# Performance work log

Measured on AMD Instinct MI355X. Metric: run time of the kernel, lower is better.

The kernel has to match this reference:

```python
import jax, jax.numpy as jnp
import numpy as np

T, H = 4096, 7168          # tokens, hidden size
Q_LORA, KV_LORA = 1536, 512
ROPE, NOPE, NH = 64, 128, 16
QK = NOPE + ROPE
MAXPOS, SLOTS = 8192, 16384
EPS = 1e-6


def _build_cos_sin_cache():
    # rotary cache layout used by the module: [max_pos, rope] = cos_half || sin_half
    half = ROPE // 2
    inv_freq = 1.0 / (10000.0 ** (np.arange(0, half, dtype=np.float32) / half))
    t = np.arange(MAXPOS, dtype=np.float32)
    freqs = np.outer(t, inv_freq)  # [MAXPOS, half]
    return jnp.asarray(np.concatenate([np.cos(freqs), np.sin(freqs)], axis=-1))


def setup_inputs() -> dict:
    key = jax.random.key(0)
    ks = jax.random.split(key, 8)
    return {
        "hidden_states": jax.random.normal(ks[0], (T, H), jnp.float32),
        "positions": jax.random.randint(ks[1], (T,), 0, MAXPOS, jnp.int32),
        "w_qkv_a": jax.random.normal(ks[2], (H, Q_LORA + KV_LORA + ROPE), jnp.float32) * 0.02,
        "q_a_ln_w": jnp.ones((Q_LORA,), jnp.float32),
        "w_q_b": jax.random.normal(ks[3], (Q_LORA, NH * QK), jnp.float32) * 0.02,
        "kv_a_ln_w": jnp.ones((KV_LORA,), jnp.float32),
        "w_kc": jax.random.normal(ks[4], (NH, NOPE, KV_LORA), jnp.float32) * 0.02,
        "cos_sin_cache": _build_cos_sin_cache(),
        "k_cache": jnp.zeros((SLOTS, KV_LORA), jnp.float32),
        "rope_cache": jnp.zeros((SLOTS, ROPE), jnp.float32),
        "slot_mapping": jnp.arange(T, dtype=jnp.int32),
    }


def _rms_norm(x, w, eps=EPS):
    return x * jax.lax.rsqrt(jnp.mean(x * x, axis=-1, keepdims=True) + eps) * w


def _interleave_rope(x, cos, sin):
    # npu_interleave_rope: de-interleave even/odd lanes into halves, then
    # apply neox-style rotation with full-dim (repeated) cos/sin.
    x1 = x[..., 0::2]
    x2 = x[..., 1::2]
    rot = jnp.concatenate([x1, x2], axis=-1)
    h = rot.shape[-1] // 2
    rot_half = jnp.concatenate([-rot[..., h:], rot[..., :h]], axis=-1)
    return rot * cos + rot_half * sin


def reference(hidden_states, positions, w_qkv_a, q_a_ln_w, w_q_b, kv_a_ln_w,
              w_kc, cos_sin_cache, k_cache, rope_cache, slot_mapping):
    # get_sin_cos: gather cache, chunk in halves, repeat each to full rope dim
    cs = cos_sin_cache[positions]                 # [T, ROPE]
    cos, sin = jnp.split(cs, 2, axis=-1)          # [T, ROPE/2] each
    cos = jnp.tile(cos, (1, 2))                   # [T, ROPE]
    sin = jnp.tile(sin, (1, 2))

    # fused qkv_a projection -> q low-rank + latent kv cache
    qkv = hidden_states @ w_qkv_a                 # [T, Q_LORA + KV_LORA + ROPE]
    q_low = qkv[:, :Q_LORA]
    latent = qkv[:, Q_LORA:]

    # q path: RMSNorm -> q_b projection -> per-head split
    q = _rms_norm(q_low, q_a_ln_w)
    q = (q @ w_q_b).reshape(-1, NH, QK)           # [T, NH, QK]
    q_nope, q_pe = q[..., :NOPE], q[..., NOPE:]

    # absorb: q_nope @ w_kc per head -> [T, NH, KV_LORA]
    q_nope = jnp.einsum("thn,hnk->thk", q_nope, w_kc)
    # interleaved rope on q_pe
    q_pe = _interleave_rope(q_pe, cos[:, None, :], sin[:, None, :])

    # kv path (npu_kv_rmsnorm_rope_cache): rmsnorm latent, rope the rope part,
    # scatter both into the paged caches at slot_mapping
    k_nope = _rms_norm(latent[:, :KV_LORA], kv_a_ln_w)     # [T, KV_LORA]
    k_rope = _interleave_rope(latent[:, KV_LORA:], cos, sin)  # [T, ROPE]
    k_cache = k_cache.at[slot_mapping].set(k_nope)
    rope_cache = rope_cache.at[slot_mapping].set(k_rope)

    q_out = jnp.concatenate([q_nope, q_pe], axis=-1)       # [T, NH, KV_LORA+ROPE]
    k_out = jnp.concatenate([k_nope, k_rope], axis=-1)     # [T, KV_LORA+ROPE]
    return q_out, k_out, k_cache, rope_cache
```

## Files before the change

kernel.cpp:

```cpp
#include <hip/hip_runtime.h>
#include <hip/hip_bf16.h>

typedef __bf16 bf16_t;
typedef __bf16 bf16x4 __attribute__((ext_vector_type(4)));
typedef __bf16 bf16x8 __attribute__((ext_vector_type(8)));
typedef float f32x4 __attribute__((ext_vector_type(4)));
typedef unsigned int uint;

#define T_TOK 4096
#define H_DIM 7168
#define QLORA 1536
#define KVLORA 512
#define ROPE_D 64
#define NOPE_D 128
#define NHEAD 16
#define NQKV 2112
#define NQB  3072
#define EPS_F 1e-6f


__global__ void cast_f32_bf16(const float* __restrict__ in, bf16_t* __restrict__ out, long n8)
{
    long stride = (long)gridDim.x * blockDim.x;
    for (long i = (long)blockIdx.x * blockDim.x + threadIdx.x; i < n8; i += stride) {
        const float4 a = ((const float4*)in)[i * 2];
        const float4 b = ((const float4*)in)[i * 2 + 1];
        bf16x8 v;
        v[0] = (bf16_t)a.x; v[1] = (bf16_t)a.y; v[2] = (bf16_t)a.z; v[3] = (bf16_t)a.w;
        v[4] = (bf16_t)b.x; v[5] = (bf16_t)b.y; v[6] = (bf16_t)b.z; v[7] = (bf16_t)b.w;
        ((bf16x8*)out)[i] = v;
    }
}

__global__ __launch_bounds__(256) void transpose_cast64(const float* __restrict__ in,
                                                        bf16_t* __restrict__ out, int R, int C)
{
    __shared__ float tile[64][65];
    const int bx = blockIdx.x * 64;
    const int by = blockIdx.y * 64;
    const int tx = threadIdx.x & 15, ty = threadIdx.x >> 4;
    #pragma unroll
    for (int i = 0; i < 4; i++) {
        const int r = ty + 16 * i;
        const float4 v = *(const float4*)&in[(long)(by + r) * C + bx + tx * 4];
        tile[r][tx * 4 + 0] = v.x; tile[r][tx * 4 + 1] = v.y;
        tile[r][tx * 4 + 2] = v.z; tile[r][tx * 4 + 3] = v.w;
    }
    __syncthreads();
    #pragma unroll
    for (int i = 0; i < 4; i++) {
        const int cc = ty + 16 * i;
        bf16x4 o;
        o[0] = (bf16_t)tile[tx * 4 + 0][cc];
        o[1] = (bf16_t)tile[tx * 4 + 1][cc];
        o[2] = (bf16_t)tile[tx * 4 + 2][cc];
        o[3] = (bf16_t)tile[tx * 4 + 3][cc];
        *(bf16x4*)&out[(long)(bx + cc) * R + by + tx * 4] = o;
    }
}

__device__ inline float block_sum_256(float v)
{
    #pragma unroll
    for (int off = 32; off > 0; off >>= 1) v += __shfl_xor(v, off, 64);
    __shared__ float tmp[4];
    __syncthreads();
    if ((threadIdx.x & 63) == 0) tmp[threadIdx.x >> 6] = v;
    __syncthreads();
    return tmp[0] + tmp[1] + tmp[2] + tmp[3];
}

__global__ __launch_bounds__(256) void rmsq_kside_kernel(
    const float* __restrict__ qkv, const float* __restrict__ qB,
    const float* __restrict__ qC, const float* __restrict__ qD,
    const float* __restrict__ q_w, const float* __restrict__ kv_w,
    const float* __restrict__ cos_sin, const int* __restrict__ positions,
    const int* __restrict__ slot_map,
    bf16_t* __restrict__ q_a, float* __restrict__ k_out,
    float* __restrict__ kc_out, float* __restrict__ rc_out)
{
    const int t = blockIdx.x;
    const long base = (long)t * NQKV;
    const float* x = qkv + base;
    const float* xB = qB ? qB + base : nullptr;
    const float* xC = qC ? qC + base : nullptr;
    const float* xD = qD ? qD + base : nullptr;

    float loc[6];
    float ss = 0.f;
    #pragma unroll
    for (int i = 0; i < 6; i++) {
        int idx = threadIdx.x + 256 * i;
        float v = x[idx];
        if (xB) v += xB[idx];
        if (xC) v += xC[idx];
        if (xD) v += xD[idx];
        loc[i] = v; ss += v * v;
    }
    ss = block_sum_256(ss);
    const float scq = rsqrtf(ss / (float)QLORA + EPS_F);
    #pragma unroll
    for (int i = 0; i < 6; i++) {
        int idx = threadIdx.x + 256 * i;
        q_a[(long)t * QLORA + idx] = (bf16_t)(loc[i] * scq * q_w[idx]);
    }

    float v0 = x[QLORA + threadIdx.x];
    float v1 = x[QLORA + threadIdx.x + 256];
    if (xB) { v0 += xB[QLORA + threadIdx.x]; v1 += xB[QLORA + threadIdx.x + 256]; }
    if (xC) { v0 += xC[QLORA + threadIdx.x]; v1 += xC[QLORA + threadIdx.x + 256]; }
    if (xD) { v0 += xD[QLORA + threadIdx.x]; v1 += xD[QLORA + threadIdx.x + 256]; }
    float ssk = v0 * v0 + v1 * v1;
    ssk = block_sum_256(ssk);
    const float sck = rsqrtf(ssk / (float)KVLORA + EPS_F);
    const int slot = slot_map[t];
    const float a0 = v0 * sck * kv_w[threadIdx.x];
    const float a1 = v1 * sck * kv_w[threadIdx.x + 256];
    k_out[(long)t * 576 + threadIdx.x]        = a0;
    k_out[(long)t * 576 + 256 + threadIdx.x]  = a1;
    kc_out[(long)slot * KVLORA + threadIdx.x]       = a0;
    kc_out[(long)slot * KVLORA + 256 + threadIdx.x] = a1;
    if (threadIdx.x < 32) {
        const int j = threadIdx.x;
        const int pos = positions[t];
        const float c = cos_sin[pos * 64 + j];
        const float s = cos_sin[pos * 64 + 32 + j];
        float x1 = x[QLORA + KVLORA + 2 * j];
        float x2 = x[QLORA + KVLORA + 2 * j + 1];
        if (xB) { x1 += xB[QLORA + KVLORA + 2 * j]; x2 += xB[QLORA + KVLORA + 2 * j + 1]; }
        if (xC) { x1 += xC[QLORA + KVLORA + 2 * j]; x2 += xC[QLORA + KVLORA + 2 * j + 1]; }
        if (xD) { x1 += xD[QLORA + KVLORA + 2 * j]; x2 += xD[QLORA + KVLORA + 2 * j + 1]; }
        const float o1 = x1 * c - x2 * s;
        const float o2 = x2 * c + x1 * s;
        k_out[(long)t * 576 + 512 + j]      = o1;
        k_out[(long)t * 576 + 512 + 32 + j] = o2;
        rc_out[(long)slot * 64 + j]      = o1;
        rc_out[(long)slot * 64 + 32 + j] = o2;
    }
}

#define GBM 128
#define GBN 128
#define GBK 64

__global__ __launch_bounds__(512) void gemm_mfma(
    const bf16_t* __restrict__ A, int lda, long sA,
    const bf16_t* __restrict__ Bt, int ldb, long sB,
    float* __restrict__ C, int ldc, long sC,
    int K, int N)
{
    __shared__ bf16_t As[2][GBM * GBK];
    __shared__ bf16_t Bs[2][GBN * GBK];

    const int nwg = gridDim.x * gridDim.y;
    const int bid = blockIdx.y * gridDim.x + blockIdx.x;
    const int cpx = nwg >> 3;
    const int swz = (bid & 7) * cpx + (bid >> 3);
    const int bx = swz % gridDim.x;
    const int by = swz / gridDim.x;

    const int tid = threadIdx.x;
    const int lane = tid & 63;
    const int w = tid >> 6;
    const int wr = w >> 2, wc = w & 3;
    const int fr = lane & 15;
    const int kg = lane >> 4;

    const long brow = (long)by * GBM;
    const long bcol = (long)bx * GBN;

    const bf16_t* Ab = A + blockIdx.z * sA + brow * lda;
    const bf16_t* Bb = Bt + blockIdx.z * sB;
    float* Cb = C + blockIdx.z * sC + brow * ldc;

    const int srow = w * 16 + (lane >> 3);
    const int scol = (((lane & 7) ^ (lane >> 3)) * 8);

    const uint rd_sw = (uint)((kg * 16) ^ ((fr & 7) << 4));
    const uint a_base = (uint)(uintptr_t)(&As[0][0]) + (uint)((wr * 64 + fr) * 128) + rd_sw;
    const uint b_base = (uint)(uintptr_t)(&Bs[0][0]) + (uint)((wc * 32 + fr) * 128) + rd_sw;

    f32x4 acc[4][2] = {};

    const int nt = K / GBK;

    auto stage = [&](int buf, int k0) {
        #pragma unroll
        for (int it = 0; it < 2; it++) {
            const int r = srow + it * 8;
            __builtin_amdgcn_global_load_lds(
                (const __attribute__((address_space(1))) void*)(Ab + (long)r * lda + k0 + scol),
                (__attribute__((address_space(3))) void*)(&As[buf][(w * 16 + it * 8) * GBK]),
                16, 0, 0);
        }
        #pragma unroll
        for (int it = 0; it < 2; it++) {
            const int r = srow + it * 8;
            long bn = bcol + r; if (bn >= N) bn = N - 1;
            __builtin_amdgcn_global_load_lds(
                (const __attribute__((address_space(1))) void*)(Bb + bn * ldb + k0 + scol),
                (__attribute__((address_space(3))) void*)(&Bs[buf][(w * 16 + it * 8) * GBK]),
                16, 0, 0);
        }
    };

    stage(0, 0);
    asm volatile("s_waitcnt vmcnt(0)" ::: "memory");
    __builtin_amdgcn_s_barrier();

    int cur = 0;
    for (int t = 0; t < nt; ++t) {
        if (t + 1 < nt) stage(cur ^ 1, (t + 1) * GBK);

        const uint aa  = a_base + (uint)(cur * (GBM * GBK * 2));
        const uint bb  = b_base + (uint)(cur * (GBN * GBK * 2));
        const uint aaX = aa ^ 64u;
        const uint bbX = bb ^ 64u;
        bf16x8 a00, a01, a02, a03, a10, a11, a12, a13, b00, b01, b10, b11;
        asm volatile("ds_read_b128 %0, %1 offset:0"    : "=v"(a00) : "v"(aa));
        asm volatile("ds_read_b128 %0, %1 offset:2048" : "=v"(a01) : "v"(aa));
        asm volatile("ds_read_b128 %0, %1 offset:4096" : "=v"(a02) : "v"(aa));
        asm volatile("ds_read_b128 %0, %1 offset:6144" : "=v"(a03) : "v"(aa));
        asm volatile("ds_read_b128 %0, %1 offset:0"    : "=v"(a10) : "v"(aaX));
        asm volatile("ds_read_b128 %0, %1 offset:2048" : "=v"(a11) : "v"(aaX));
        asm volatile("ds_read_b128 %0, %1 offset:4096" : "=v"(a12) : "v"(aaX));
        asm volatile("ds_read_b128 %0, %1 offset:6144" : "=v"(a13) : "v"(aaX));
        asm volatile("ds_read_b128 %0, %1 offset:0"    : "=v"(b00) : "v"(bb));
        asm volatile("ds_read_b128 %0, %1 offset:2048" : "=v"(b01) : "v"(bb));
        asm volatile("ds_read_b128 %0, %1 offset:0"    : "=v"(b10) : "v"(bbX));
        asm volatile("ds_read_b128 %0, %1 offset:2048" : "=v"(b11) : "v"(bbX));
        asm volatile("s_waitcnt lgkmcnt(0)" ::: "memory");
        __builtin_amdgcn_sched_barrier(0);

        acc[0][0] = __builtin_amdgcn_mfma_f32_16x16x32_bf16(a00, b00, acc[0][0], 0, 0, 0);
        acc[0][1] = __builtin_amdgcn_mfma_f32_16x16x32_bf16(a00, b01, acc[0][1], 0, 0, 0);
        acc[1][0] = __builtin_amdgcn_mfma_f32_16x16x32_bf16(a01, b00, acc[1][0], 0, 0, 0);
        acc[1][1] = __builtin_amdgcn_mfma_f32_16x16x32_bf16(a01, b01, acc[1][1], 0, 0, 0);
        acc[2][0] = __builtin_amdgcn_mfma_f32_16x16x32_bf16(a02, b00, acc[2][0], 0, 0, 0);
        acc[2][1] = __builtin_amdgcn_mfma_f32_16x16x32_bf16(a02, b01, acc[2][1], 0, 0, 0);
        acc[3][0] = __builtin_amdgcn_mfma_f32_16x16x32_bf16(a03, b00, acc[3][0], 0, 0, 0);
        acc[3][1] = __builtin_amdgcn_mfma_f32_16x16x32_bf16(a03, b01, acc[3][1], 0, 0, 0);
        acc[0][0] = __builtin_amdgcn_mfma_f32_16x16x32_bf16(a10, b10, acc[0][0], 0, 0, 0);
        acc[0][1] = __builtin_amdgcn_mfma_f32_16x16x32_bf16(a10, b11, acc[0][1], 0, 0, 0);
        acc[1][0] = __builtin_amdgcn_mfma_f32_16x16x32_bf16(a11, b10, acc[1][0], 0, 0, 0);
        acc[1][1] = __builtin_amdgcn_mfma_f32_16x16x32_bf16(a11, b11, acc[1][1], 0, 0, 0);
        acc[2][0] = __builtin_amdgcn_mfma_f32_16x16x32_bf16(a12, b10, acc[2][0], 0, 0, 0);
        acc[2][1] = __builtin_amdgcn_mfma_f32_16x16x32_bf16(a12, b11, acc[2][1], 0, 0, 0);
        acc[3][0] = __builtin_amdgcn_mfma_f32_16x16x32_bf16(a13, b10, acc[3][0], 0, 0, 0);
        acc[3][1] = __builtin_amdgcn_mfma_f32_16x16x32_bf16(a13, b11, acc[3][1], 0, 0, 0);

        asm volatile("s_waitcnt vmcnt(0)" ::: "memory");
        __builtin_amdgcn_s_barrier();
        cur ^= 1;
    }

    #pragma unroll
    for (int i = 0; i < 4; i++) {
        #pragma unroll
        for (int j = 0; j < 2; j++) {
            const int row0 = wr * 64 + i * 16 + kg * 4;
            const long col = bcol + wc * 32 + j * 16 + fr;
            if (col < N) {
                #pragma unroll
                for (int r = 0; r < 4; r++)
                    Cb[(long)(row0 + r) * ldc + col] = acc[i][j][r];
            }
        }
    }
}

__global__ __launch_bounds__(512) void gemm2_fused(
    const bf16_t* __restrict__ A,
    const bf16_t* __restrict__ Bt,
    const float* __restrict__ cos_sin,
    const int* __restrict__ positions,
    bf16_t* __restrict__ q_nope,
    float* __restrict__ q_out)
{
    __shared__ bf16_t As[2][GBM * GBK];
    __shared__ bf16_t Bs[2][GBN * GBK];

    const int nwg = gridDim.x * gridDim.y;
    const int bid = blockIdx.y * gridDim.x + blockIdx.x;
    const int cpx = nwg >> 3;
    const int swz = (bid & 7) * cpx + (bid >> 3);
    const int bx = swz % gridDim.x;
    const int by = swz / gridDim.x;

    const int tid = threadIdx.x;
    const int lane = tid & 63;
    const int w = tid >> 6;
    const int wr = w >> 2, wc = w & 3;
    const int fr = lane & 15;
    const int kg = lane >> 4;

    const int brow = by * GBM;
    const int bcol = bx * GBN;

    const bf16_t* Ab = A + (long)brow * QLORA;
    const bf16_t* Bb = Bt + (long)bcol * QLORA;

    const int srow = w * 16 + (lane >> 3);
    const int scol = (((lane & 7) ^ (lane >> 3)) * 8);

    const uint rd_sw = (uint)((kg * 16) ^ ((fr & 7) << 4));
    const uint a_base = (uint)(uintptr_t)(&As[0][0]) + (uint)((wr * 64 + fr) * 128) + rd_sw;
    const uint b_base = (uint)(uintptr_t)(&Bs[0][0]) + (uint)((wc * 32 + fr) * 128) + rd_sw;

    f32x4 acc[4][2] = {};

    const int nt = QLORA / GBK;

    auto stage = [&](int buf, int k0) {
        #pragma unroll
        for (int it = 0; it < 2; it++) {
            const int r = srow + it * 8;
            __builtin_amdgcn_global_load_lds(
                (const __attribute__((address_space(1))) void*)(Ab + (long)r * QLORA + k0 + scol),
                (__attribute__((address_space(3))) void*)(&As[buf][(w * 16 + it * 8) * GBK]),
                16, 0, 0);
            __builtin_amdgcn_global_load_lds(
                (const __attribute__((address_space(1))) void*)(Bb + (long)r * QLORA + k0 + scol),
                (__attribute__((address_space(3))) void*)(&Bs[buf][(w * 16 + it * 8) * GBK]),
                16, 0, 0);
        }
    };

    stage(0, 0);
    asm volatile("s_waitcnt vmcnt(0)" ::: "memory");
    __builtin_amdgcn_s_barrier();

    int cur = 0;
    for (int t = 0; t < nt; ++t) {
        if (t + 1 < nt) stage(cur ^ 1, (t + 1) * GBK);

        const uint aa  = a_base + (uint)(cur * (GBM * GBK * 2));
        const uint bb  = b_base + (uint)(cur * (GBN * GBK * 2));
        const uint aaX = aa ^ 64u;
        const uint bbX = bb ^ 64u;
        bf16x8 a00, a01, a02, a03, a10, a11, a12, a13, b00, b01, b10, b11;
        asm volatile("ds_read_b128 %0, %1 offset:0"    : "=v"(a00) : "v"(aa));
        asm volatile("ds_read_b128 %0, %1 offset:2048" : "=v"(a01) : "v"(aa));
        asm volatile("ds_read_b128 %0, %1 offset:4096" : "=v"(a02) : "v"(aa));
        asm volatile("ds_read_b128 %0, %1 offset:6144" : "=v"(a03) : "v"(aa));
        asm volatile("ds_read_b128 %0, %1 offset:0"    : "=v"(a10) : "v"(aaX));
        asm volatile("ds_read_b128 %0, %1 offset:2048" : "=v"(a11) : "v"(aaX));
        asm volatile("ds_read_b128 %0, %1 offset:4096" : "=v"(a12) : "v"(aaX));
        asm volatile("ds_read_b128 %0, %1 offset:6144" : "=v"(a13) : "v"(aaX));
        asm volatile("ds_read_b128 %0, %1 offset:0"    : "=v"(b00) : "v"(bb));
        asm volatile("ds_read_b128 %0, %1 offset:2048" : "=v"(b01) : "v"(bb));
        asm volatile("ds_read_b128 %0, %1 offset:0"    : "=v"(b10) : "v"(bbX));
        asm volatile("ds_read_b128 %0, %1 offset:2048" : "=v"(b11) : "v"(bbX));
        asm volatile("s_waitcnt lgkmcnt(0)" ::: "memory");
        __builtin_amdgcn_sched_barrier(0);

        acc[0][0] = __builtin_amdgcn_mfma_f32_16x16x32_bf16(a00, b00, acc[0][0], 0, 0, 0);
        acc[0][1] = __builtin_amdgcn_mfma_f32_16x16x32_bf16(a00, b01, acc[0][1], 0, 0, 0);
        acc[1][0] = __builtin_amdgcn_mfma_f32_16x16x32_bf16(a01, b00, acc[1][0], 0, 0, 0);
        acc[1][1] = __builtin_amdgcn_mfma_f32_16x16x32_bf16(a01, b01, acc[1][1], 0, 0, 0);
        acc[2][0] = __builtin_amdgcn_mfma_f32_16x16x32_bf16(a02, b00, acc[2][0], 0, 0, 0);
        acc[2][1] = __builtin_amdgcn_mfma_f32_16x16x32_bf16(a02, b01, acc[2][1], 0, 0, 0);
        acc[3][0] = __builtin_amdgcn_mfma_f32_16x16x32_bf16(a03, b00, acc[3][0], 0, 0, 0);
        acc[3][1] = __builtin_amdgcn_mfma_f32_16x16x32_bf16(a03, b01, acc[3][1], 0, 0, 0);
        acc[0][0] = __builtin_amdgcn_mfma_f32_16x16x32_bf16(a10, b10, acc[0][0], 0, 0, 0);
        acc[0][1] = __builtin_amdgcn_mfma_f32_16x16x32_bf16(a10, b11, acc[0][1], 0, 0, 0);
        acc[1][0] = __builtin_amdgcn_mfma_f32_16x16x32_bf16(a11, b10, acc[1][0], 0, 0, 0);
        acc[1][1] = __builtin_amdgcn_mfma_f32_16x16x32_bf16(a11, b11, acc[1][1], 0, 0, 0);
        acc[2][0] = __builtin_amdgcn_mfma_f32_16x16x32_bf16(a12, b10, acc[2][0], 0, 0, 0);
        acc[2][1] = __builtin_amdgcn_mfma_f32_16x16x32_bf16(a12, b11, acc[2][1], 0, 0, 0);
        acc[3][0] = __builtin_amdgcn_mfma_f32_16x16x32_bf16(a13, b10, acc[3][0], 0, 0, 0);
        acc[3][1] = __builtin_amdgcn_mfma_f32_16x16x32_bf16(a13, b11, acc[3][1], 0, 0, 0);

        asm volatile("s_waitcnt vmcnt(0)" ::: "memory");
        __builtin_amdgcn_s_barrier();
        cur ^= 1;
    }

    #pragma unroll
    for (int i = 0; i < 4; i++) {
        #pragma unroll
        for (int j = 0; j < 2; j++) {
            const int row0 = wr * 64 + i * 16 + kg * 4;
            const int col  = bcol + wc * 32 + j * 16 + fr;
            const int h  = col / 192;
            const int jj = col - h * 192;
            if (jj < 128) {
                #pragma unroll
                for (int r = 0; r < 4; r++) {
                    const int t = brow + row0 + r;
                    q_nope[((long)h * T_TOK + t) * NOPE_D + jj] = (bf16_t)acc[i][j][r];
                }
            } else {
                const int idx = jj - 128;
                const int j2 = idx >> 1;
                const int odd = idx & 1;
                #pragma unroll
                for (int r = 0; r < 4; r++) {
                    const int t = brow + row0 + r;
                    const float v = acc[i][j][r];
                    const float p = __shfl_xor(v, 1, 64);
                    const int pos = positions[t];
                    const float c = cos_sin[pos * 64 + j2];
                    const float s = cos_sin[pos * 64 + 32 + j2];
                    const float o = odd ? (v * c + p * s) : (v * c - p * s);
                    q_out[(long)t * 9216 + h * 576 + 512 + (odd ? 32 : 0) + j2] = o;
                }
            }
        }
    }
}

__global__ __launch_bounds__(512) void gemm3_k128(
    const bf16_t* __restrict__ A,
    const bf16_t* __restrict__ Bt,
    float* __restrict__ C)
{
    __shared__ bf16_t As[2][GBM * GBK];
    __shared__ bf16_t Bs[2][GBN * GBK];

    const int nwg = gridDim.x * gridDim.y;
    const int bid = blockIdx.y * gridDim.x + blockIdx.x;
    const int cpx = nwg >> 3;
    const int swz = (bid & 7) * cpx + (bid >> 3);
    const int bx = swz % gridDim.x;
    const int by = swz / gridDim.x;

    const int tid = threadIdx.x;
    const int lane = tid & 63;
    const int w = tid >> 6;
    const int wr = w >> 2, wc = w & 3;
    const int fr = lane & 15;
    const int kg = lane >> 4;

    const long brow = (long)by * GBM;
    const long bcol = (long)bx * GBN;

    const bf16_t* Ab = A + (long)blockIdx.z * T_TOK * NOPE_D + brow * NOPE_D;
    const bf16_t* Bb = Bt + blockIdx.z * 128;
    float* Cb = C + blockIdx.z * 576 + brow * 9216;

    const int srow = w * 16 + (lane >> 3);
    const int scol = (((lane & 7) ^ (lane >> 3)) * 8);

    const uint rd_sw = (uint)((kg * 16) ^ ((fr & 7) << 4));

    #pragma unroll
    for (int kh = 0; kh < 2; kh++) {
        #pragma unroll
        for (int it = 0; it < 2; it++) {
            const int r = srow + it * 8;
            __builtin_amdgcn_global_load_lds(
                (const __attribute__((address_space(1))) void*)(Ab + (long)r * NOPE_D + kh * 64 + scol),
                (__attribute__((address_space(3))) void*)(&As[kh][(w * 16 + it * 8) * GBK]),
                16, 0, 0);
        }
        #pragma unroll
        for (int it = 0; it < 2; it++) {
            const int r = srow + it * 8;
            __builtin_amdgcn_global_load_lds(
                (const __attribute__((address_space(1))) void*)(Bb + (bcol + r) * 2048 + kh * 64 + scol),
                (__attribute__((address_space(3))) void*)(&Bs[kh][(w * 16 + it * 8) * GBK]),
                16, 0, 0);
        }
    }
    asm volatile("s_waitcnt vmcnt(0)" ::: "memory");
    __builtin_amdgcn_s_barrier();

    f32x4 acc[4][2] = {};

    #pragma unroll
    for (int kh = 0; kh < 2; kh++) {
        const uint aa  = (uint)(uintptr_t)(&As[kh][0]) + (uint)((wr * 64 + fr) * 128) + rd_sw;
        const uint bb  = (uint)(uintptr_t)(&Bs[kh][0]) + (uint)((wc * 32 + fr) * 128) + rd_sw;
        const uint aaX = aa ^ 64u;
        const uint bbX = bb ^ 64u;
        bf16x8 a00, a01, a02, a03, a10, a11, a12, a13, b00, b01, b10, b11;
        asm volatile("ds_read_b128 %0, %1 offset:0"    : "=v"(a00) : "v"(aa));
        asm volatile("ds_read_b128 %0, %1 offset:2048" : "=v"(a01) : "v"(aa));
        asm volatile("ds_read_b128 %0, %1 offset:4096" : "=v"(a02) : "v"(aa));
        asm volatile("ds_read_b128 %0, %1 offset:6144" : "=v"(a03) : "v"(aa));
        asm volatile("ds_read_b128 %0, %1 offset:0"    : "=v"(a10) : "v"(aaX));
        asm volatile("ds_read_b128 %0, %1 offset:2048" : "=v"(a11) : "v"(aaX));
        asm volatile("ds_read_b128 %0, %1 offset:4096" : "=v"(a12) : "v"(aaX));
        asm volatile("ds_read_b128 %0, %1 offset:6144" : "=v"(a13) : "v"(aaX));
        asm volatile("ds_read_b128 %0, %1 offset:0"    : "=v"(b00) : "v"(bb));
        asm volatile("ds_read_b128 %0, %1 offset:2048" : "=v"(b01) : "v"(bb));
        asm volatile("ds_read_b128 %0, %1 offset:0"    : "=v"(b10) : "v"(bbX));
        asm volatile("ds_read_b128 %0, %1 offset:2048" : "=v"(b11) : "v"(bbX));
        asm volatile("s_waitcnt lgkmcnt(0)" ::: "memory");
        __builtin_amdgcn_sched_barrier(0);

        acc[0][0] = __builtin_amdgcn_mfma_f32_16x16x32_bf16(a00, b00, acc[0][0], 0, 0, 0);
        acc[0][1] = __builtin_amdgcn_mfma_f32_16x16x32_bf16(a00, b01, acc[0][1], 0, 0, 0);
        acc[1][0] = __builtin_amdgcn_mfma_f32_16x16x32_bf16(a01, b00, acc[1][0], 0, 0, 0);
        acc[1][1] = __builtin_amdgcn_mfma_f32_16x16x32_bf16(a01, b01, acc[1][1], 0, 0, 0);
        acc[2][0] = __builtin_amdgcn_mfma_f32_16x16x32_bf16(a02, b00, acc[2][0], 0, 0, 0);
        acc[2][1] = __builtin_amdgcn_mfma_f32_16x16x32_bf16(a02, b01, acc[2][1], 0, 0, 0);
        acc[3][0] = __builtin_amdgcn_mfma_f32_16x16x32_bf16(a03, b00, acc[3][0], 0, 0, 0);
        acc[3][1] = __builtin_amdgcn_mfma_f32_16x16x32_bf16(a03, b01, acc[3][1], 0, 0, 0);
        acc[0][0] = __builtin_amdgcn_mfma_f32_16x16x32_bf16(a10, b10, acc[0][0], 0, 0, 0);
        acc[0][1] = __builtin_amdgcn_mfma_f32_16x16x32_bf16(a10, b11, acc[0][1], 0, 0, 0);
        acc[1][0] = __builtin_amdgcn_mfma_f32_16x16x32_bf16(a11, b10, acc[1][0], 0, 0, 0);
        acc[1][1] = __builtin_amdgcn_mfma_f32_16x16x32_bf16(a11, b11, acc[1][1], 0, 0, 0);
        acc[2][0] = __builtin_amdgcn_mfma_f32_16x16x32_bf16(a12, b10, acc[2][0], 0, 0, 0);
        acc[2][1] = __builtin_amdgcn_mfma_f32_16x16x32_bf16(a12, b11, acc[2][1], 0, 0, 0);
        acc[3][0] = __builtin_amdgcn_mfma_f32_16x16x32_bf16(a13, b10, acc[3][0], 0, 0, 0);
        acc[3][1] = __builtin_amdgcn_mfma_f32_16x16x32_bf16(a13, b11, acc[3][1], 0, 0, 0);
    }

    #pragma unroll
    for (int i = 0; i < 4; i++) {
        #pragma unroll
        for (int j = 0; j < 2; j++) {
            const int row0 = wr * 64 + i * 16 + kg * 4;
            const long col = bcol + wc * 32 + j * 16 + fr;
            #pragma unroll
            for (int r = 0; r < 4; r++)
                Cb[(long)(row0 + r) * 9216 + col] = acc[i][j][r];
        }
    }
}


extern "C" void kernel_launch(void* const* d_in, const int* in_sizes, int n_in,
                              void* d_out, int out_size, void* d_ws, size_t ws_size,
                              hipStream_t stream)
{
    const float* hs       = (const float*)d_in[0];
    const int*   positions= (const int*)d_in[1];
    const float* w_qkv_a  = (const float*)d_in[2];
    const float* q_a_ln_w = (const float*)d_in[3];
    const float* w_q_b    = (const float*)d_in[4];
    const float* kv_a_ln_w= (const float*)d_in[5];
    const float* w_kc     = (const float*)d_in[6];
    const float* cos_sin  = (const float*)d_in[7];
    const float* k_cache_in  = (const float*)d_in[8];
    const float* rope_cache_in = (const float*)d_in[9];
    const int*   slot_map = (const int*)d_in[10];

    float* out   = (float*)d_out;
    float* q_out = out;
    float* k_out = out + 37748736;
    float* kc_out = out + 40108032;
    float* rc_out = out + 48496640;

    char* ws = (char*)d_ws;
    bf16_t* hs_bf  = (bf16_t*)(ws + 0);
    bf16_t* wqkvaT = (bf16_t*)(ws + 58720256);
    bf16_t* wqbT   = (bf16_t*)(ws + 88997888);
    bf16_t* wkcT   = (bf16_t*)(ws + 98435072);
    float*  qkv0   = (float*)(ws + 100532224);

    int splitk = 1;
    if (ws_size >= (size_t)238944256) splitk = 4;
    else if (ws_size >= (size_t)169738240) splitk = 2;

    float* qkv1 = nullptr; float* qkv2 = nullptr; float* qkv3 = nullptr;
    bf16_t* q_a;
    bf16_t* q_nope;
    if (splitk >= 2) {
        qkv1   = (float*)(ws + 135135232);
        q_a    = (bf16_t*)(ws + 0);
        q_nope = (bf16_t*)(ws + 135135232);
        if (splitk == 4) {
            qkv2 = (float*)(ws + 169738240);
            qkv3 = (float*)(ws + 204341248);
        }
    } else {
        q_a    = (bf16_t*)(ws + 135135232);
        q_nope = (bf16_t*)(ws + 100532224);
    }

    hipMemcpyAsync(kc_out, k_cache_in, (size_t)16384 * 512 * 4, hipMemcpyDeviceToDevice, stream);
    hipMemcpyAsync(rc_out, rope_cache_in, (size_t)16384 * 64 * 4, hipMemcpyDeviceToDevice, stream);

    cast_f32_bf16<<<2048, 256, 0, stream>>>(hs, hs_bf, (long)T_TOK * H_DIM / 8);
    transpose_cast64<<<dim3(NQKV / 64, H_DIM / 64), 256, 0, stream>>>(w_qkv_a, wqkvaT, H_DIM, NQKV);
    transpose_cast64<<<dim3(NQB / 64, QLORA / 64), 256, 0, stream>>>(w_q_b, wqbT, QLORA, NQB);
    transpose_cast64<<<dim3(512 / 64, 2048 / 64), 256, 0, stream>>>(w_kc, wkcT, 2048, 512);

    {
        const int kslice = H_DIM / splitk;
        gemm_mfma<<<dim3((NQKV + GBN - 1) / GBN, T_TOK / GBM, splitk), 512, 0, stream>>>(
            hs_bf, H_DIM, kslice, wqkvaT, H_DIM, kslice,
            qkv0, NQKV, (long)T_TOK * NQKV, kslice, NQKV);
    }

    rmsq_kside_kernel<<<T_TOK, 256, 0, stream>>>(qkv0, qkv1, qkv2, qkv3,
                                                 q_a_ln_w, kv_a_ln_w,
                                                 cos_sin, positions, slot_map,
                                                 q_a, k_out, kc_out, rc_out);

    gemm2_fused<<<dim3(NQB / GBN, T_TOK / GBM), 512, 0, stream>>>(
        q_a, wqbT, cos_sin, positions, q_nope, q_out);

    gemm3_k128<<<dim3(KVLORA / GBN, T_TOK / GBM, NHEAD), 512, 0, stream>>>(
        q_nope, wkcT, q_out);
}
```

Before: 373.5 us.

## Use intra-block K-split wave pairs with 64x64 warp tiles in GEMMs

The QKV and q_b GEMMs now have each wave pair split the K=64 tile: both waves own a 64x64 output quadrant, and each takes half the K dimension. Partial sums are reduced through LDS before the epilogue. This gives a larger per-wave MFMA tile with fewer LDS reads per FLOP. Global split-K for the first GEMM is capped at 2, which drops the 4-way partial buffers from the RMSNorm kernel. The trade-offs are more accumulator registers (launch bounds now hint 4 blocks), an extra LDS reduction and barrier, and less parallelism for the first GEMM when the workspace would have allowed split 4.

```diff
diff --git a/kernel.cpp b/kernel.cpp
--- a/kernel.cpp
+++ b/kernel.cpp
@@ -72,7 +72,6 @@
 
 __global__ __launch_bounds__(256) void rmsq_kside_kernel(
     const float* __restrict__ qkv, const float* __restrict__ qB,
-    const float* __restrict__ qC, const float* __restrict__ qD,
     const float* __restrict__ q_w, const float* __restrict__ kv_w,
     const float* __restrict__ cos_sin, const int* __restrict__ positions,
     const int* __restrict__ slot_map,
@@ -83,8 +82,6 @@
     const long base = (long)t * NQKV;
     const float* x = qkv + base;
     const float* xB = qB ? qB + base : nullptr;
-    const float* xC = qC ? qC + base : nullptr;
-    const float* xD = qD ? qD + base : nullptr;
 
     float loc[6];
     float ss = 0.f;
@@ -93,8 +90,6 @@
         int idx = threadIdx.x + 256 * i;
         float v = x[idx];
         if (xB) v += xB[idx];
-        if (xC) v += xC[idx];
-        if (xD) v += xD[idx];
         loc[i] = v; ss += v * v;
     }
     ss = block_sum_256(ss);
@@ -108,8 +103,6 @@
     float v0 = x[QLORA + threadIdx.x];
     float v1 = x[QLORA + threadIdx.x + 256];
     if (xB) { v0 += xB[QLORA + threadIdx.x]; v1 += xB[QLORA + threadIdx.x + 256]; }
-    if (xC) { v0 += xC[QLORA + threadIdx.x]; v1 += xC[QLORA + threadIdx.x + 256]; }
-    if (xD) { v0 += xD[QLORA + threadIdx.x]; v1 += xD[QLORA + threadIdx.x + 256]; }
     float ssk = v0 * v0 + v1 * v1;
     ssk = block_sum_256(ssk);
     const float sck = rsqrtf(ssk / (float)KVLORA + EPS_F);
@@ -128,8 +121,6 @@
         float x1 = x[QLORA + KVLORA + 2 * j];
         float x2 = x[QLORA + KVLORA + 2 * j + 1];
         if (xB) { x1 += xB[QLORA + KVLORA + 2 * j]; x2 += xB[QLORA + KVLORA + 2 * j + 1]; }
-        if (xC) { x1 += xC[QLORA + KVLORA + 2 * j]; x2 += xC[QLORA + KVLORA + 2 * j + 1]; }
-        if (xD) { x1 += xD[QLORA + KVLORA + 2 * j]; x2 += xD[QLORA + KVLORA + 2 * j + 1]; }
         const float o1 = x1 * c - x2 * s;
         const float o2 = x2 * c + x1 * s;
         k_out[(long)t * 576 + 512 + j]      = o1;
@@ -143,7 +134,36 @@
 #define GBN 128
 #define GBK 64
 
-__global__ __launch_bounds__(512) void gemm_mfma(
+#define KSPLIT_TILE_COMPUTE(aa, bb)                                                          \
+    bf16x8 a0, a1, a2, a3, b0, b1, b2, b3;                                                   \
+    asm volatile("ds_read_b128 %0, %1 offset:0"    : "=v"(a0) : "v"(aa));                    \
+    asm volatile("ds_read_b128 %0, %1 offset:2048" : "=v"(a1) : "v"(aa));                    \
+    asm volatile("ds_read_b128 %0, %1 offset:4096" : "=v"(a2) : "v"(aa));                    \
+    asm volatile("ds_read_b128 %0, %1 offset:6144" : "=v"(a3) : "v"(aa));                    \
+    asm volatile("ds_read_b128 %0, %1 offset:0"    : "=v"(b0) : "v"(bb));                    \
+    asm volatile("ds_read_b128 %0, %1 offset:2048" : "=v"(b1) : "v"(bb));                    \
+    asm volatile("ds_read_b128 %0, %1 offset:4096" : "=v"(b2) : "v"(bb));                    \
+    asm volatile("ds_read_b128 %0, %1 offset:6144" : "=v"(b3) : "v"(bb));                    \
+    asm volatile("s_waitcnt lgkmcnt(0)" ::: "memory");                                       \
+    __builtin_amdgcn_sched_barrier(0);                                                       \
+    acc[0][0] = __builtin_amdgcn_mfma_f32_16x16x32_bf16(a0, b0, acc[0][0], 0, 0, 0);         \
+    acc[0][1] = __builtin_amdgcn_mfma_f32_16x16x32_bf16(a0, b1, acc[0][1], 0, 0, 0);         \
+    acc[0][2] = __builtin_amdgcn_mfma_f32_16x16x32_bf16(a0, b2, acc[0][2], 0, 0, 0);         \
+    acc[0][3] = __builtin_amdgcn_mfma_f32_16x16x32_bf16(a0, b3, acc[0][3], 0, 0, 0);         \
+    acc[1][0] = __builtin_amdgcn_mfma_f32_16x16x32_bf16(a1, b0, acc[1][0], 0, 0, 0);         \
+    acc[1][1] = __builtin_amdgcn_mfma_f32_16x16x32_bf16(a1, b1, acc[1][1], 0, 0, 0);         \
+    acc[1][2] = __builtin_amdgcn_mfma_f32_16x16x32_bf16(a1, b2, acc[1][2], 0, 0, 0);         \
+    acc[1][3] = __builtin_amdgcn_mfma_f32_16x16x32_bf16(a1, b3, acc[1][3], 0, 0, 0);         \
+    acc[2][0] = __builtin_amdgcn_mfma_f32_16x16x32_bf16(a2, b0, acc[2][0], 0, 0, 0);         \
+    acc[2][1] = __builtin_amdgcn_mfma_f32_16x16x32_bf16(a2, b1, acc[2][1], 0, 0, 0);         \
+    acc[2][2] = __builtin_amdgcn_mfma_f32_16x16x32_bf16(a2, b2, acc[2][2], 0, 0, 0);         \
+    acc[2][3] = __builtin_amdgcn_mfma_f32_16x16x32_bf16(a2, b3, acc[2][3], 0, 0, 0);         \
+    acc[3][0] = __builtin_amdgcn_mfma_f32_16x16x32_bf16(a3, b0, acc[3][0], 0, 0, 0);         \
+    acc[3][1] = __builtin_amdgcn_mfma_f32_16x16x32_bf16(a3, b1, acc[3][1], 0, 0, 0);         \
+    acc[3][2] = __builtin_amdgcn_mfma_f32_16x16x32_bf16(a3, b2, acc[3][2], 0, 0, 0);         \
+    acc[3][3] = __builtin_amdgcn_mfma_f32_16x16x32_bf16(a3, b3, acc[3][3], 0, 0, 0);
+
+__global__ __launch_bounds__(512, 4) void gemm_mfma(
     const bf16_t* __restrict__ A, int lda, long sA,
     const bf16_t* __restrict__ Bt, int ldb, long sB,
     float* __restrict__ C, int ldc, long sC,
@@ -162,7 +182,9 @@
     const int tid = threadIdx.x;
     const int lane = tid & 63;
     const int w = tid >> 6;
-    const int wr = w >> 2, wc = w & 3;
+    const int q = w >> 1;
+    const int p = w & 1;
+    const int qr = q >> 1, qc = q & 1;
     const int fr = lane & 15;
     const int kg = lane >> 4;
 
@@ -176,11 +198,11 @@
     const int srow = w * 16 + (lane >> 3);
     const int scol = (((lane & 7) ^ (lane >> 3)) * 8);
 
-    const uint rd_sw = (uint)((kg * 16) ^ ((fr & 7) << 4));
-    const uint a_base = (uint)(uintptr_t)(&As[0][0]) + (uint)((wr * 64 + fr) * 128) + rd_sw;
-    const uint b_base = (uint)(uintptr_t)(&Bs[0][0]) + (uint)((wc * 32 + fr) * 128) + rd_sw;
-
-    f32x4 acc[4][2] = {};
+    const uint rd_sw = (uint)(((kg * 16) ^ ((fr & 7) << 4)) ^ (p << 6));
+    const uint a_base = (uint)(uintptr_t)(&As[0][0]) + (uint)((qr * 64 + fr) * 128) + rd_sw;
+    const uint b_base = (uint)(uintptr_t)(&Bs[0][0]) + (uint)((qc * 64 + fr) * 128) + rd_sw;
+
+    f32x4 acc[4][4] = {};
 
     const int nt = K / GBK;
 
@@ -212,64 +234,44 @@
     for (int t = 0; t < nt; ++t) {
         if (t + 1 < nt) stage(cur ^ 1, (t + 1) * GBK);
 
-        const uint aa  = a_base + (uint)(cur * (GBM * GBK * 2));
-        const uint bb  = b_base + (uint)(cur * (GBN * GBK * 2));
-        const uint aaX = aa ^ 64u;
-        const uint bbX = bb ^ 64u;
-        bf16x8 a00, a01, a02, a03, a10, a11, a12, a13, b00, b01, b10, b11;
-        asm volatile("ds_read_b128 %0, %1 offset:0"    : "=v"(a00) : "v"(aa));
-        asm volatile("ds_read_b128 %0, %1 offset:2048" : "=v"(a01) : "v"(aa));
-        asm volatile("ds_read_b128 %0, %1 offset:4096" : "=v"(a02) : "v"(aa));
-        asm volatile("ds_read_b128 %0, %1 offset:6144" : "=v"(a03) : "v"(aa));
-        asm volatile("ds_read_b128 %0, %1 offset:0"    : "=v"(a10) : "v"(aaX));
-        asm volatile("ds_read_b128 %0, %1 offset:2048" : "=v"(a11) : "v"(aaX));
-        asm volatile("ds_read_b128 %0, %1 offset:4096" : "=v"(a12) : "v"(aaX));
-        asm volatile("ds_read_b128 %0, %1 offset:6144" : "=v"(a13) : "v"(aaX));
-        asm volatile("ds_read_b128 %0, %1 offset:0"    : "=v"(b00) : "v"(bb));
-        asm volatile("ds_read_b128 %0, %1 offset:2048" : "=v"(b01) : "v"(bb));
-        asm volatile("ds_read_b128 %0, %1 offset:0"    : "=v"(b10) : "v"(bbX));
-        asm volatile("ds_read_b128 %0, %1 offset:2048" : "=v"(b11) : "v"(bbX));
-        asm volatile("s_waitcnt lgkmcnt(0)" ::: "memory");
-        __builtin_amdgcn_sched_barrier(0);
-
-        acc[0][0] = __builtin_amdgcn_mfma_f32_16x16x32_bf16(a00, b00, acc[0][0], 0, 0, 0);
-        acc[0][1] = __builtin_amdgcn_mfma_f32_16x16x32_bf16(a00, b01, acc[0][1], 0, 0, 0);
-        acc[1][0] = __builtin_amdgcn_mfma_f32_16x16x32_bf16(a01, b00, acc[1][0], 0, 0, 0);
-        acc[1][1] = __builtin_amdgcn_mfma_f32_16x16x32_bf16(a01, b01, acc[1][1], 0, 0, 0);
-        acc[2][0] = __builtin_amdgcn_mfma_f32_16x16x32_bf16(a02, b00, acc[2][0], 0, 0, 0);
-        acc[2][1] = __builtin_amdgcn_mfma_f32_16x16x32_bf16(a02, b01, acc[2][1], 0, 0, 0);
-        acc[3][0] = __builtin_amdgcn_mfma_f32_16x16x32_bf16(a03, b00, acc[3][0], 0, 0, 0);
-        acc[3][1] = __builtin_amdgcn_mfma_f32_16x16x32_bf16(a03, b01, acc[3][1], 0, 0, 0);
-        acc[0][0] = __builtin_amdgcn_mfma_f32_16x16x32_bf16(a10, b10, acc[0][0], 0, 0, 0);
-        acc[0][1] = __builtin_amdgcn_mfma_f32_16x16x32_bf16(a10, b11, acc[0][1], 0, 0, 0);
-        acc[1][0] = __builtin_amdgcn_mfma_f32_16x16x32_bf16(a11, b10, acc[1][0], 0, 0, 0);
-        acc[1][1] = __builtin_amdgcn_mfma_f32_16x16x32_bf16(a11, b11, acc[1][1], 0, 0, 0);
-        acc[2][0] = __builtin_amdgcn_mfma_f32_16x16x32_bf16(a12, b10, acc[2][0], 0, 0, 0);
-        acc[2][1] = __builtin_amdgcn_mfma_f32_16x16x32_bf16(a12, b11, acc[2][1], 0, 0, 0);
-        acc[3][0] = __builtin_amdgcn_mfma_f32_16x16x32_bf16(a13, b10, acc[3][0], 0, 0, 0);
-        acc[3][1] = __builtin_amdgcn_mfma_f32_16x16x32_bf16(a13, b11, acc[3][1], 0, 0, 0);
+        const uint aa = a_base + (uint)(cur * (GBM * GBK * 2));
+        const uint bb = b_base + (uint)(cur * (GBN * GBK * 2));
+        { KSPLIT_TILE_COMPUTE(aa, bb) }
 
         asm volatile("s_waitcnt vmcnt(0)" ::: "memory");
         __builtin_amdgcn_s_barrier();
         cur ^= 1;
     }
 
-    #pragma unroll
-    for (int i = 0; i < 4; i++) {
-        #pragma unroll
-        for (int j = 0; j < 2; j++) {
-            const int row0 = wr * 64 + i * 16 + kg * 4;
-            const long col = bcol + wc * 32 + j * 16 + fr;
-            if (col < N) {
-                #pragma unroll
-                for (int r = 0; r < 4; r++)
-                    Cb[(long)(row0 + r) * ldc + col] = acc[i][j][r];
+    float* red = (q < 2) ? (float*)&As[0][0] : (float*)&Bs[0][0];
+    red += (q & 1) * 4096;
+    if (p == 1) {
+        #pragma unroll
+        for (int i = 0; i < 4; i++)
+            #pragma unroll
+            for (int j = 0; j < 4; j++)
+                *(f32x4*)&red[(i * 4 + j) * 256 + lane * 4] = acc[i][j];
+    }
+    __syncthreads();
+    if (p == 0) {
+        #pragma unroll
+        for (int i = 0; i < 4; i++) {
+            #pragma unroll
+            for (int j = 0; j < 4; j++) {
+                acc[i][j] += *(const f32x4*)&red[(i * 4 + j) * 256 + lane * 4];
+                const int row0 = qr * 64 + i * 16 + kg * 4;
+                const long col = bcol + qc * 64 + j * 16 + fr;
+                if (col < N) {
+                    #pragma unroll
+                    for (int r = 0; r < 4; r++)
+                        Cb[(long)(row0 + r) * ldc + col] = acc[i][j][r];
+                }
             }
         }
     }
 }
 
-__global__ __launch_bounds__(512) void gemm2_fused(
+__global__ __launch_bounds__(512, 4) void gemm2_fused(
     const bf16_t* __restrict__ A,
     const bf16_t* __restrict__ Bt,
     const float* __restrict__ cos_sin,
@@ -290,7 +292,9 @@
     const int tid = threadIdx.x;
     const int lane = tid & 63;
     const int w = tid >> 6;
-    const int wr = w >> 2, wc = w & 3;
+    const int q = w >> 1;
+    const int p = w & 1;
+    const int qr = q >> 1, qc = q & 1;
     const int fr = lane & 15;
     const int kg = lane >> 4;
 
@@ -303,11 +307,11 @@
     const int srow = w * 16 + (lane >> 3);
     const int scol = (((lane & 7) ^ (lane >> 3)) * 8);
 
-    const uint rd_sw = (uint)((kg * 16) ^ ((fr & 7) << 4));
-    const uint a_base = (uint)(uintptr_t)(&As[0][0]) + (uint)((wr * 64 + fr) * 128) + rd_sw;
-    const uint b_base = (uint)(uintptr_t)(&Bs[0][0]) + (uint)((wc * 32 + fr) * 128) + rd_sw;
-
-    f32x4 acc[4][2] = {};
+    const uint rd_sw = (uint)(((kg * 16) ^ ((fr & 7) << 4)) ^ (p << 6));
+    const uint a_base = (uint)(uintptr_t)(&As[0][0]) + (uint)((qr * 64 + fr) * 128) + rd_sw;
+    const uint b_base = (uint)(uintptr_t)(&Bs[0][0]) + (uint)((qc * 64 + fr) * 128) + rd_sw;
+
+    f32x4 acc[4][4] = {};
 
     const int nt = QLORA / GBK;
 
@@ -334,76 +338,56 @@
     for (int t = 0; t < nt; ++t) {
         if (t + 1 < nt) stage(cur ^ 1, (t + 1) * GBK);
 
-        const uint aa  = a_base + (uint)(cur * (GBM * GBK * 2));
-        const uint bb  = b_base + (uint)(cur * (GBN * GBK * 2));
-        const uint aaX = aa ^ 64u;
-        const uint bbX = bb ^ 64u;
-        bf16x8 a00, a01, a02, a03, a10, a11, a12, a13, b00, b01, b10, b11;
-        asm volatile("ds_read_b128 %0, %1 offset:0"    : "=v"(a00) : "v"(aa));
-        asm volatile("ds_read_b128 %0, %1 offset:2048" : "=v"(a01) : "v"(aa));
-        asm volatile("ds_read_b128 %0, %1 offset:4096" : "=v"(a02) : "v"(aa));
-        asm volatile("ds_read_b128 %0, %1 offset:6144" : "=v"(a03) : "v"(aa));
-        asm volatile("ds_read_b128 %0, %1 offset:0"    : "=v"(a10) : "v"(aaX));
-        asm volatile("ds_read_b128 %0, %1 offset:2048" : "=v"(a11) : "v"(aaX));
-        asm volatile("ds_read_b128 %0, %1 offset:4096" : "=v"(a12) : "v"(aaX));
-        asm volatile("ds_read_b128 %0, %1 offset:6144" : "=v"(a13) : "v"(aaX));
-        asm volatile("ds_read_b128 %0, %1 offset:0"    : "=v"(b00) : "v"(bb));
-        asm volatile("ds_read_b128 %0, %1 offset:2048" : "=v"(b01) : "v"(bb));
-        asm volatile("ds_read_b128 %0, %1 offset:0"    : "=v"(b10) : "v"(bbX));
-        asm volatile("ds_read_b128 %0, %1 offset:2048" : "=v"(b11) : "v"(bbX));
-        asm volatile("s_waitcnt lgkmcnt(0)" ::: "memory");
-        __builtin_amdgcn_sched_barrier(0);
-
-        acc[0][0] = __builtin_amdgcn_mfma_f32_16x16x32_bf16(a00, b00, acc[0][0], 0, 0, 0);
-        acc[0][1] = __builtin_amdgcn_mfma_f32_16x16x32_bf16(a00, b01, acc[0][1], 0, 0, 0);
-        acc[1][0] = __builtin_amdgcn_mfma_f32_16x16x32_bf16(a01, b00, acc[1][0], 0, 0, 0);
-        acc[1][1] = __builtin_amdgcn_mfma_f32_16x16x32_bf16(a01, b01, acc[1][1], 0, 0, 0);
-        acc[2][0] = __builtin_amdgcn_mfma_f32_16x16x32_bf16(a02, b00, acc[2][0], 0, 0, 0);
-        acc[2][1] = __builtin_amdgcn_mfma_f32_16x16x32_bf16(a02, b01, acc[2][1], 0, 0, 0);
-        acc[3][0] = __builtin_amdgcn_mfma_f32_16x16x32_bf16(a03, b00, acc[3][0], 0, 0, 0);
-        acc[3][1] = __builtin_amdgcn_mfma_f32_16x16x32_bf16(a03, b01, acc[3][1], 0, 0, 0);
-        acc[0][0] = __builtin_amdgcn_mfma_f32_16x16x32_bf16(a10, b10, acc[0][0], 0, 0, 0);
-        acc[0][1] = __builtin_amdgcn_mfma_f32_16x16x32_bf16(a10, b11, acc[0][1], 0, 0, 0);
-        acc[1][0] = __builtin_amdgcn_mfma_f32_16x16x32_bf16(a11, b10, acc[1][0], 0, 0, 0);
-        acc[1][1] = __builtin_amdgcn_mfma_f32_16x16x32_bf16(a11, b11, acc[1][1], 0, 0, 0);
-        acc[2][0] = __builtin_amdgcn_mfma_f32_16x16x32_bf16(a12, b10, acc[2][0], 0, 0, 0);
-        acc[2][1] = __builtin_amdgcn_mfma_f32_16x16x32_bf16(a12, b11, acc[2][1], 0, 0, 0);
-        acc[3][0] = __builtin_amdgcn_mfma_f32_16x16x32_bf16(a13, b10, acc[3][0], 0, 0, 0);
-        acc[3][1] = __builtin_amdgcn_mfma_f32_16x16x32_bf16(a13, b11, acc[3][1], 0, 0, 0);
+        const uint aa = a_base + (uint)(cur * (GBM * GBK * 2));
+        const uint bb = b_base + (uint)(cur * (GBN * GBK * 2));
+        { KSPLIT_TILE_COMPUTE(aa, bb) }
 
         asm volatile("s_waitcnt vmcnt(0)" ::: "memory");
         __builtin_amdgcn_s_barrier();
         cur ^= 1;
     }
 
-    #pragma unroll
-    for (int i = 0; i < 4; i++) {
-        #pragma unroll
-        for (int j = 0; j < 2; j++) {
-            const int row0 = wr * 64 + i * 16 + kg * 4;
-            const int col  = bcol + wc * 32 + j * 16 + fr;
-            const int h  = col / 192;
-            const int jj = col - h * 192;
-            if (jj < 128) {
-                #pragma unroll
-                for (int r = 0; r < 4; r++) {
-                    const int t = brow + row0 + r;
-                    q_nope[((long)h * T_TOK + t) * NOPE_D + jj] = (bf16_t)acc[i][j][r];
-                }
-            } else {
-                const int idx = jj - 128;
-                const int j2 = idx >> 1;
-                const int odd = idx & 1;
-                #pragma unroll
-                for (int r = 0; r < 4; r++) {
-                    const int t = brow + row0 + r;
-                    const float v = acc[i][j][r];
-                    const float p = __shfl_xor(v, 1, 64);
-                    const int pos = positions[t];
-                    const float c = cos_sin[pos * 64 + j2];
-                    const float s = cos_sin[pos * 64 + 32 + j2];
-                    const float o = odd ? (v * c + p * s) : (v * c - p * s);
-                    q_out[(long)t * 9216 + h * 576 + 512 + (odd ? 32 : 0) + j2] = o;
+    float* red = (q < 2) ? (float*)&As[0][0] : (float*)&Bs[0][0];
+    red += (q & 1) * 4096;
+    if (p == 1) {
+        #pragma unroll
+        for (int i = 0; i < 4; i++)
+            #pragma unroll
+            for (int j = 0; j < 4; j++)
+                *(f32x4*)&red[(i * 4 + j) * 256 + lane * 4] = acc[i][j];
+    }
+    __syncthreads();
+    if (p == 0) {
+        #pragma unroll
+        for (int i = 0; i < 4; i++) {
+            #pragma unroll
+            for (int j = 0; j < 4; j++) {
+                acc[i][j] += *(const f32x4*)&red[(i * 4 + j) * 256 + lane * 4];
+                const int row0 = qr * 64 + i * 16 + kg * 4;
+                const int col  = bcol + qc * 64 + j * 16 + fr;
+                const int h  = col / 192;
+                const int jj = col - h * 192;
+                if (jj < 128) {
+                    #pragma unroll
+                    for (int r = 0; r < 4; r++) {
+                        const int t = brow + row0 + r;
+                        q_nope[((long)h * T_TOK + t) * NOPE_D + jj] = (bf16_t)acc[i][j][r];
+                    }
+                } else {
+                    const int idx = jj - 128;
+                    const int j2 = idx >> 1;
+                    const int odd = idx & 1;
+                    #pragma unroll
+                    for (int r = 0; r < 4; r++) {
+                        const int t = brow + row0 + r;
+                        const float v = acc[i][j][r];
+                        const float pr = __shfl_xor(v, 1, 64);
+                        const int pos = positions[t];
+                        const float c = cos_sin[pos * 64 + j2];
+                        const float s = cos_sin[pos * 64 + 32 + j2];
+                        const float o = odd ? (v * c + pr * s) : (v * c - pr * s);
+                        q_out[(long)t * 9216 + h * 576 + 512 + (odd ? 32 : 0) + j2] = o;
+                    }
                 }
             }
         }
@@ -551,21 +535,15 @@
     bf16_t* wkcT   = (bf16_t*)(ws + 98435072);
     float*  qkv0   = (float*)(ws + 100532224);
 
-    int splitk = 1;
-    if (ws_size >= (size_t)238944256) splitk = 4;
-    else if (ws_size >= (size_t)169738240) splitk = 2;
-
-    float* qkv1 = nullptr; float* qkv2 = nullptr; float* qkv3 = nullptr;
+    const bool splitk = ws_size >= (size_t)169738240;
+
+    float* qkv1 = nullptr;
     bf16_t* q_a;
     bf16_t* q_nope;
-    if (splitk >= 2) {
+    if (splitk) {
         qkv1   = (float*)(ws + 135135232);
         q_a    = (bf16_t*)(ws + 0);
         q_nope = (bf16_t*)(ws + 135135232);
-        if (splitk == 4) {
-            qkv2 = (float*)(ws + 169738240);
-            qkv3 = (float*)(ws + 204341248);
-        }
     } else {
         q_a    = (bf16_t*)(ws + 135135232);
         q_nope = (bf16_t*)(ws + 100532224);
@@ -579,15 +557,16 @@
     transpose_cast64<<<dim3(NQB / 64, QLORA / 64), 256, 0, stream>>>(w_q_b, wqbT, QLORA, NQB);
     transpose_cast64<<<dim3(512 / 64, 2048 / 64), 256, 0, stream>>>(w_kc, wkcT, 2048, 512);
 
-    {
-        const int kslice = H_DIM / splitk;
-        gemm_mfma<<<dim3((NQKV + GBN - 1) / GBN, T_TOK / GBM, splitk), 512, 0, stream>>>(
-            hs_bf, H_DIM, kslice, wqkvaT, H_DIM, kslice,
-            qkv0, NQKV, (long)T_TOK * NQKV, kslice, NQKV);
-    }
-
-    rmsq_kside_kernel<<<T_TOK, 256, 0, stream>>>(qkv0, qkv1, qkv2, qkv3,
-                                                 q_a_ln_w, kv_a_ln_w,
+    if (splitk) {
+        gemm_mfma<<<dim3((NQKV + GBN - 1) / GBN, T_TOK / GBM, 2), 512, 0, stream>>>(
+            hs_bf, H_DIM, 3584, wqkvaT, H_DIM, 3584,
+            qkv0, NQKV, (long)T_TOK * NQKV, 3584, NQKV);
+    } else {
+        gemm_mfma<<<dim3((NQKV + GBN - 1) / GBN, T_TOK / GBM, 1), 512, 0, stream>>>(
+            hs_bf, H_DIM, 0, wqkvaT, H_DIM, 0, qkv0, NQKV, 0, H_DIM, NQKV);
+    }
+
+    rmsq_kside_kernel<<<T_TOK, 256, 0, stream>>>(qkv0, qkv1, q_a_ln_w, kv_a_ln_w,
                                                  cos_sin, positions, slot_map,
                                                  q_a, k_out, kc_out, rc_out);
 
```

After: 362.4 us. 3.0% less time.
